# Kernel tuning notes

Measured on AMD Instinct MI355X. Metric: run time of the kernel, lower is better.

Reference implementation:

```python
import jax, jax.numpy as jnp
import numpy as np

N_TRIALS, T, N, IN_DIM = 32, 2048, 512, 64
DT = 0.1


def setup_inputs() -> dict:
    key = jax.random.key(0)
    k1, k2, k3, k4, k5 = jax.random.split(key, 5)
    inp = jax.random.normal(k1, (N_TRIALS, T, IN_DIM), dtype=jnp.float32)
    noise = jax.random.normal(k2, (N_TRIALS, T, N), dtype=jnp.float32)
    J = jax.random.normal(k3, (N, N), dtype=jnp.float32) * (1.0 / np.sqrt(N))  # init_std/sqrt(N)
    B = jax.random.normal(k4, (N, IN_DIM), dtype=jnp.float32)
    sig = jax.random.uniform(k5, (N,), dtype=jnp.float32, minval=0.1, maxval=1.0)
    W = jnp.eye(N, dtype=jnp.float32)  # module sets W = torch.eye(N)
    return {"inp": inp, "noise": noise, "J": J, "B": B, "sig": sig, "W": W}


def reference(inp, noise, J, B, sig, W):
    n_trials = inp.shape[0]
    n = J.shape[0]
    x0 = jnp.zeros((n_trials, n), dtype=inp.dtype)  # initial_state=None -> zeros
    sqdt = DT ** 0.5
    sig2 = sig * sig
    inp_t = jnp.swapaxes(inp, 0, 1)      # (T, n_trials, input_dim)
    noise_t = jnp.swapaxes(noise, 0, 1)  # (T, n_trials, N)

    def step(x, ue):
        u, eps = ue
        x_new = (1.0 - DT) * x + DT * (jnp.tanh(x) @ J.T + u @ B.T) + sqdt * (eps * sig2)
        y = jnp.tanh(x_new) @ W
        return x_new, (x_new, y)

    _, (xs, ys) = jax.lax.scan(step, x0, (inp_t, noise_t))
    x_seq = jnp.concatenate([x0[:, None, :], jnp.swapaxes(xs, 0, 1)], axis=1)  # (n_trials, T+1, N)
    output_seq = jnp.swapaxes(ys, 0, 1)  # (n_trials, T, N)
    return x_seq, output_seq
```

## Files before the change

kernel.cpp:

```cpp
#include <hip/hip_runtime.h>
#include <stdint.h>


#define T_STEPS 2048
#define N_NEUR  512
#define IN_DIM  64

typedef __attribute__((ext_vector_type(8))) short bf16x8;
typedef __attribute__((ext_vector_type(4))) short short4v;
typedef __attribute__((ext_vector_type(4))) float f32x4;

__device__ __forceinline__ short f2bf(float x) {
    union { float f; uint32_t u; } v; v.f = x;
    uint32_t r = v.u + 0x7fffu + ((v.u >> 16) & 1u);
    return (short)(r >> 16);
}
__device__ __forceinline__ float bf2f(short s) {
    union { float f; uint32_t u; } v;
    v.u = ((uint32_t)(uint16_t)s) << 16;
    return v.f;
}

__device__ __forceinline__ int th_idx(int trial, int k) {
    int byte = trial * 1024 + k * 2;
    byte ^= (trial & 7) << 4;
    return byte >> 1;
}
__device__ __forceinline__ int u_idx(int trial, int d) {
    int byte = trial * 128 + d * 2;
    byte ^= (trial & 7) << 4;
    return byte >> 1;
}

__launch_bounds__(256, 1)
__global__ void rnn_main(const float* __restrict__ inp,
                         const float* __restrict__ noise,
                         const float* __restrict__ Jm,
                         const float* __restrict__ Bm,
                         const float* __restrict__ sig,
                         float* __restrict__ out_x,
                         float* __restrict__ out_y,
                         uint64_t* __restrict__ xch)
{
    const int tid  = threadIdx.x;
    const int lane = tid & 63;
    const int w    = tid >> 6;
    const int s    = blockIdx.x & 7;
    const int h    = blockIdx.x >> 3;
    const int i0   = s * 4;
    const int nbase = h * 256 + w * 64;
    const int li   = lane & 15;
    const int lk   = lane >> 4;

    __shared__ short th[16 * 512];
    __shared__ short uhi[16 * 64];
    __shared__ short ulo[16 * 64];

    {
        bf16x8 z = {0,0,0,0,0,0,0,0};
        for (int j = tid; j < (16*512)/8; j += 256) *(bf16x8*)&th[j*8] = z;
        for (int j = tid; j < (16*64)/8;  j += 256) { *(bf16x8*)&uhi[j*8] = z; *(bf16x8*)&ulo[j*8] = z; }
    }

    bf16x8 Jf[4][16];
    #pragma unroll
    for (int mt = 0; mt < 4; ++mt) {
        const float* rowp = Jm + (size_t)(nbase + 16*mt + li) * N_NEUR;
        #pragma unroll
        for (int kt = 0; kt < 16; ++kt) {
            const float* p = rowp + kt*32 + lk*8;
            f32x4 a = *(const f32x4*)p;
            f32x4 b = *(const f32x4*)(p + 4);
            bf16x8 f;
            f[0]=f2bf(a[0]); f[1]=f2bf(a[1]); f[2]=f2bf(a[2]); f[3]=f2bf(a[3]);
            f[4]=f2bf(b[0]); f[5]=f2bf(b[1]); f[6]=f2bf(b[2]); f[7]=f2bf(b[3]);
            Jf[mt][kt] = f;
        }
    }

    bf16x8 Bhi[4][2], Blo[4][2];
    #pragma unroll
    for (int mt = 0; mt < 4; ++mt) {
        const float* rowp = Bm + (size_t)(nbase + 16*mt + li) * IN_DIM;
        #pragma unroll
        for (int kt2 = 0; kt2 < 2; ++kt2) {
            const float* p = rowp + kt2*32 + lk*8;
            f32x4 a = *(const f32x4*)p;
            f32x4 b = *(const f32x4*)(p + 4);
            bf16x8 fh, fl;
            #pragma unroll
            for (int e = 0; e < 4; ++e) {
                short hi = f2bf(a[e]); fh[e]   = hi; fl[e]   = f2bf(a[e] - bf2f(hi));
                short h2 = f2bf(b[e]); fh[e+4] = h2; fl[e+4] = f2bf(b[e] - bf2f(h2));
            }
            Bhi[mt][kt2] = fh; Blo[mt][kt2] = fl;
        }
    }

    const float SQDT = 0.316227766016837933f;
    f32x4 s2[4];
    #pragma unroll
    for (int mt = 0; mt < 4; ++mt) {
        int n4 = nbase + 16*mt + lk*4;
        #pragma unroll
        for (int r = 0; r < 4; ++r) { float sg = sig[n4 + r]; s2[mt][r] = SQDT * sg * sg; }
    }

    f32x4 x[4];
    #pragma unroll
    for (int mt = 0; mt < 4; ++mt) x[mt] = f32x4{0.f,0.f,0.f,0.f};

    const bool act  = (li < 4);
    const int trial = i0 + li;
    const int i_stage = tid >> 6;
    const int d_stage = tid & 63;

    {
        float v = inp[((size_t)(i0 + i_stage) * T_STEPS + 0) * IN_DIM + d_stage];
        short hi = f2bf(v);
        short lo = f2bf(v - bf2f(hi));
        uhi[u_idx(i_stage, d_stage)] = hi;
        ulo[u_idx(i_stage, d_stage)] = lo;
    }
    f32x4 noise_cur[4];
    #pragma unroll
    for (int mt = 0; mt < 4; ++mt) noise_cur[mt] = f32x4{0.f,0.f,0.f,0.f};
    if (act) {
        #pragma unroll
        for (int mt = 0; mt < 4; ++mt) {
            int n4 = nbase + 16*mt + lk*4;
            noise_cur[mt] = *(const f32x4*)&noise[((size_t)trial * T_STEPS + 0) * N_NEUR + n4];
        }
    }
    __syncthreads();

    for (int t = 0; t < T_STEPS; ++t) {
        const bool more = (t < T_STEPS - 1);

        float inp_next = 0.f;
        f32x4 noise_next[4];
        if (more) {
            inp_next = inp[((size_t)(i0 + i_stage) * T_STEPS + (t+1)) * IN_DIM + d_stage];
            if (act) {
                #pragma unroll
                for (int mt = 0; mt < 4; ++mt) {
                    int n4 = nbase + 16*mt + lk*4;
                    noise_next[mt] = *(const f32x4*)&noise[((size_t)trial * T_STEPS + (t+1)) * N_NEUR + n4];
                }
            }
        }

        f32x4 acc[4];
        #pragma unroll
        for (int mt = 0; mt < 4; ++mt) acc[mt] = f32x4{0.f,0.f,0.f,0.f};

        #pragma unroll
        for (int kt2 = 0; kt2 < 2; ++kt2) {
            bf16x8 uh = *(const bf16x8*)&uhi[u_idx(li, kt2*32 + lk*8)];
            bf16x8 ul = *(const bf16x8*)&ulo[u_idx(li, kt2*32 + lk*8)];
            #pragma unroll
            for (int mt = 0; mt < 4; ++mt) {
                acc[mt] = __builtin_amdgcn_mfma_f32_16x16x32_bf16(Bhi[mt][kt2], uh, acc[mt], 0, 0, 0);
                acc[mt] = __builtin_amdgcn_mfma_f32_16x16x32_bf16(Blo[mt][kt2], uh, acc[mt], 0, 0, 0);
                acc[mt] = __builtin_amdgcn_mfma_f32_16x16x32_bf16(Bhi[mt][kt2], ul, acc[mt], 0, 0, 0);
            }
        }
        #pragma unroll
        for (int kt = 0; kt < 16; ++kt) {
            bf16x8 bf = *(const bf16x8*)&th[th_idx(li, kt*32 + lk*8)];
            #pragma unroll
            for (int mt = 0; mt < 4; ++mt)
                acc[mt] = __builtin_amdgcn_mfma_f32_16x16x32_bf16(Jf[mt][kt], bf, acc[mt], 0, 0, 0);
        }

        __syncthreads();

        const uint32_t tag = (uint32_t)(t + 1);
        const uint64_t tag2 = ((uint64_t)tag << 32) | ((uint64_t)tag << 48);
        uint64_t* own_slot = xch + ((((t & 1) * 16) + s*2 + h) << 9);

        #pragma unroll
        for (int mt = 0; mt < 4; ++mt) {
            int n4 = nbase + 16*mt + lk*4;
            f32x4 xn, tv;
            #pragma unroll
            for (int r = 0; r < 4; ++r) {
                xn[r] = 0.9f * x[mt][r] + 0.1f * acc[mt][r] + noise_cur[mt][r] * s2[mt][r];
                float e = __expf(2.0f * xn[r]);
                tv[r] = 1.0f - 2.0f / (e + 1.0f);
            }
            x[mt] = xn;
            if (act) {
                *(f32x4*)&out_x[((size_t)trial * (T_STEPS+1) + (t+1)) * N_NEUR + n4] = xn;
                *(f32x4*)&out_y[((size_t)trial * T_STEPS + t) * N_NEUR + n4] = tv;
                short4v pk;
                pk[0]=f2bf(tv[0]); pk[1]=f2bf(tv[1]); pk[2]=f2bf(tv[2]); pk[3]=f2bf(tv[3]);
                *(short4v*)&th[th_idx(li, n4)] = pk;
                if (more) {
                    int nl = n4 - h*256;
                    uint64_t w0 = (uint64_t)(uint16_t)pk[0] | ((uint64_t)(uint16_t)pk[1] << 16) | tag2;
                    uint64_t w1 = (uint64_t)(uint16_t)pk[2] | ((uint64_t)(uint16_t)pk[3] << 16) | tag2;
                    uint64_t* dst = own_slot + li*128 + (nl >> 1);
                    __hip_atomic_store(dst,     w0, __ATOMIC_RELAXED, __HIP_MEMORY_SCOPE_AGENT);
                    __hip_atomic_store(dst + 1, w1, __ATOMIC_RELAXED, __HIP_MEMORY_SCOPE_AGENT);
                }
            }
        }

        if (more) {
            {
                short hi = f2bf(inp_next);
                short lo = f2bf(inp_next - bf2f(hi));
                uhi[u_idx(i_stage, d_stage)] = hi;
                ulo[u_idx(i_stage, d_stage)] = lo;
            }
            {
                const uint64_t* src = xch + ((((t & 1) * 16) + s*2 + (h^1)) << 9)
                                          + i_stage*128 + d_stage*2;
                const uint32_t want_hi = tag | (tag << 16);
                uint64_t w0, w1;
                for (;;) {
                    w0 = __hip_atomic_load(src,     __ATOMIC_RELAXED, __HIP_MEMORY_SCOPE_AGENT);
                    w1 = __hip_atomic_load(src + 1, __ATOMIC_RELAXED, __HIP_MEMORY_SCOPE_AGENT);
                    if ((uint32_t)(w0 >> 32) == want_hi && (uint32_t)(w1 >> 32) == want_hi) break;
                    __builtin_amdgcn_s_sleep(1);
                }
                short4v pv;
                pv[0] = (short)(w0 & 0xffff); pv[1] = (short)((w0 >> 16) & 0xffff);
                pv[2] = (short)(w1 & 0xffff); pv[3] = (short)((w1 >> 16) & 0xffff);
                *(short4v*)&th[th_idx(i_stage, (h^1)*256 + d_stage*4)] = pv;
            }
            #pragma unroll
            for (int mt = 0; mt < 4; ++mt) noise_cur[mt] = noise_next[mt];
            __syncthreads();
        }
    }
}

__global__ void init_kernel(float* __restrict__ out_x, uint64_t* __restrict__ xch) {
    int tid = blockIdx.x * 256 + threadIdx.x;
    if (tid < 2*8*2*512)
        __hip_atomic_store(&xch[tid], 0ull, __ATOMIC_RELAXED, __HIP_MEMORY_SCOPE_AGENT);
    if (tid < 32 * N_NEUR) {
        int i = tid >> 9;
        int n = tid & 511;
        out_x[(size_t)i * ((size_t)(T_STEPS+1) * N_NEUR) + n] = 0.0f;
    }
}

extern "C" void kernel_launch(void* const* d_in, const int* in_sizes, int n_in,
                              void* d_out, int out_size, void* d_ws, size_t ws_size,
                              hipStream_t stream) {
    const float* inp   = (const float*)d_in[0];
    const float* noise = (const float*)d_in[1];
    const float* Jm    = (const float*)d_in[2];
    const float* Bm    = (const float*)d_in[3];
    const float* sig   = (const float*)d_in[4];

    float* out_x = (float*)d_out;
    float* out_y = out_x + (size_t)32 * (T_STEPS+1) * N_NEUR;

    uint64_t* xch = (uint64_t*)d_ws;

    init_kernel<<<64, 256, 0, stream>>>(out_x, xch);
    rnn_main<<<16, 256, 0, stream>>>(inp, noise, Jm, Bm, sig, out_x, out_y, xch);
}
```

Before: 6.072 ms.

## Repartition RNN across 8-block trial groups with double-buffered LDS exchange

Changes the work split so each block handles all 16 trials of one group for a 64-neuron slice, with 8 blocks per group exchanging tanh activations through tagged global slots. Previously each block covered 4 trials and 256 neurons, and 12 of the 16 MFMA columns were padding. The new split uses all 16 MFMA columns, cuts per-wave MFMA count and register-held J to a quarter, and double-buffers the shared th/u arrays to remove one barrier per step. In exchange, each step now needs a 7-way all-gather across blocks instead of a 2-way exchange, which raises synchronization latency and global traffic on the serial critical path.

```diff
diff --git a/kernel.cpp b/kernel.cpp
--- a/kernel.cpp
+++ b/kernel.cpp
@@ -30,6 +30,13 @@
     int byte = trial * 128 + d * 2;
     byte ^= (trial & 7) << 4;
     return byte >> 1;
+}
+
+__device__ __forceinline__ uint64_t aload(const uint64_t* p) {
+    return __hip_atomic_load(p, __ATOMIC_RELAXED, __HIP_MEMORY_SCOPE_AGENT);
+}
+__device__ __forceinline__ void astore(uint64_t* p, uint64_t v) {
+    __hip_atomic_store(p, v, __ATOMIC_RELAXED, __HIP_MEMORY_SCOPE_AGENT);
 }
 
 __launch_bounds__(256, 1)
@@ -44,28 +51,28 @@
 {
     const int tid  = threadIdx.x;
     const int lane = tid & 63;
-    const int w    = tid >> 6;
-    const int s    = blockIdx.x & 7;
-    const int h    = blockIdx.x >> 3;
-    const int i0   = s * 4;
-    const int nbase = h * 256 + w * 64;
+    const int wv   = tid >> 6;
+    const int g    = blockIdx.x >> 3;
+    const int slo  = blockIdx.x & 7;
     const int li   = lane & 15;
     const int lk   = lane >> 4;
-
-    __shared__ short th[16 * 512];
-    __shared__ short uhi[16 * 64];
-    __shared__ short ulo[16 * 64];
+    const int n0   = slo * 64 + wv * 16;
+    const int trial = g * 16 + li;
+    const int n4   = n0 + lk * 4;
+
+    __shared__ short th[2][16 * 512];
+    __shared__ short uhi[2][16 * 64];
+    __shared__ short ulo[2][16 * 64];
 
     {
         bf16x8 z = {0,0,0,0,0,0,0,0};
-        for (int j = tid; j < (16*512)/8; j += 256) *(bf16x8*)&th[j*8] = z;
-        for (int j = tid; j < (16*64)/8;  j += 256) { *(bf16x8*)&uhi[j*8] = z; *(bf16x8*)&ulo[j*8] = z; }
-    }
-
-    bf16x8 Jf[4][16];
-    #pragma unroll
-    for (int mt = 0; mt < 4; ++mt) {
-        const float* rowp = Jm + (size_t)(nbase + 16*mt + li) * N_NEUR;
+        short* thp = &th[0][0];
+        for (int j = tid; j < (2*16*512)/8; j += 256) *(bf16x8*)&thp[j*8] = z;
+    }
+
+    bf16x8 Jf[16];
+    {
+        const float* rowp = Jm + (size_t)(n0 + li) * N_NEUR;
         #pragma unroll
         for (int kt = 0; kt < 16; ++kt) {
             const float* p = rowp + kt*32 + lk*8;
@@ -74,14 +81,13 @@
             bf16x8 f;
             f[0]=f2bf(a[0]); f[1]=f2bf(a[1]); f[2]=f2bf(a[2]); f[3]=f2bf(a[3]);
             f[4]=f2bf(b[0]); f[5]=f2bf(b[1]); f[6]=f2bf(b[2]); f[7]=f2bf(b[3]);
-            Jf[mt][kt] = f;
-        }
-    }
-
-    bf16x8 Bhi[4][2], Blo[4][2];
-    #pragma unroll
-    for (int mt = 0; mt < 4; ++mt) {
-        const float* rowp = Bm + (size_t)(nbase + 16*mt + li) * IN_DIM;
+            Jf[kt] = f;
+        }
+    }
+
+    bf16x8 Bhi[2], Blo[2];
+    {
+        const float* rowp = Bm + (size_t)(n0 + li) * IN_DIM;
         #pragma unroll
         for (int kt2 = 0; kt2 < 2; ++kt2) {
             const float* p = rowp + kt2*32 + lk*8;
@@ -90,157 +96,152 @@
             bf16x8 fh, fl;
             #pragma unroll
             for (int e = 0; e < 4; ++e) {
-                short hi = f2bf(a[e]); fh[e]   = hi; fl[e]   = f2bf(a[e] - bf2f(hi));
+                short h1 = f2bf(a[e]); fh[e]   = h1; fl[e]   = f2bf(a[e] - bf2f(h1));
                 short h2 = f2bf(b[e]); fh[e+4] = h2; fl[e+4] = f2bf(b[e] - bf2f(h2));
             }
-            Bhi[mt][kt2] = fh; Blo[mt][kt2] = fl;
+            Bhi[kt2] = fh; Blo[kt2] = fl;
         }
     }
 
     const float SQDT = 0.316227766016837933f;
-    f32x4 s2[4];
+    f32x4 s2;
     #pragma unroll
-    for (int mt = 0; mt < 4; ++mt) {
-        int n4 = nbase + 16*mt + lk*4;
-        #pragma unroll
-        for (int r = 0; r < 4; ++r) { float sg = sig[n4 + r]; s2[mt][r] = SQDT * sg * sg; }
-    }
-
-    f32x4 x[4];
-    #pragma unroll
-    for (int mt = 0; mt < 4; ++mt) x[mt] = f32x4{0.f,0.f,0.f,0.f};
-
-    const bool act  = (li < 4);
-    const int trial = i0 + li;
-    const int i_stage = tid >> 6;
-    const int d_stage = tid & 63;
-
-    {
-        float v = inp[((size_t)(i0 + i_stage) * T_STEPS + 0) * IN_DIM + d_stage];
-        short hi = f2bf(v);
-        short lo = f2bf(v - bf2f(hi));
-        uhi[u_idx(i_stage, d_stage)] = hi;
-        ulo[u_idx(i_stage, d_stage)] = lo;
-    }
-    f32x4 noise_cur[4];
-    #pragma unroll
-    for (int mt = 0; mt < 4; ++mt) noise_cur[mt] = f32x4{0.f,0.f,0.f,0.f};
-    if (act) {
-        #pragma unroll
-        for (int mt = 0; mt < 4; ++mt) {
-            int n4 = nbase + 16*mt + lk*4;
-            noise_cur[mt] = *(const f32x4*)&noise[((size_t)trial * T_STEPS + 0) * N_NEUR + n4];
-        }
-    }
+    for (int r = 0; r < 4; ++r) { float sg = sig[n4 + r]; s2[r] = SQDT * sg * sg; }
+
+    f32x4 x = f32x4{0.f, 0.f, 0.f, 0.f};
+
+    const int it  = tid >> 4;
+    const int c16 = tid & 15;
+    const int d4  = c16 * 4;
+
+    {
+        f32x4 uv = *(const f32x4*)&inp[((size_t)(g*16 + it) * T_STEPS + 0) * IN_DIM + d4];
+        short4v h, l;
+        #pragma unroll
+        for (int e = 0; e < 4; ++e) { h[e] = f2bf(uv[e]); l[e] = f2bf(uv[e] - bf2f(h[e])); }
+        *(short4v*)&uhi[0][u_idx(it, d4)] = h;
+        *(short4v*)&ulo[0][u_idx(it, d4)] = l;
+    }
+    f32x4 noise_cur = *(const f32x4*)&noise[((size_t)trial * T_STEPS + 0) * N_NEUR + n4];
     __syncthreads();
 
     for (int t = 0; t < T_STEPS; ++t) {
         const bool more = (t < T_STEPS - 1);
-
-        float inp_next = 0.f;
-        f32x4 noise_next[4];
-        if (more) {
-            inp_next = inp[((size_t)(i0 + i_stage) * T_STEPS + (t+1)) * IN_DIM + d_stage];
-            if (act) {
-                #pragma unroll
-                for (int mt = 0; mt < 4; ++mt) {
-                    int n4 = nbase + 16*mt + lk*4;
-                    noise_next[mt] = *(const f32x4*)&noise[((size_t)trial * T_STEPS + (t+1)) * N_NEUR + n4];
-                }
-            }
-        }
-
-        f32x4 acc[4];
-        #pragma unroll
-        for (int mt = 0; mt < 4; ++mt) acc[mt] = f32x4{0.f,0.f,0.f,0.f};
-
+        const int rp = t & 1, wp = rp ^ 1, par = t & 1;
+
+        f32x4 inp_next = f32x4{0.f,0.f,0.f,0.f};
+        f32x4 noise_next = f32x4{0.f,0.f,0.f,0.f};
+        if (more) {
+            inp_next = *(const f32x4*)&inp[((size_t)(g*16 + it) * T_STEPS + (t+1)) * IN_DIM + d4];
+            noise_next = *(const f32x4*)&noise[((size_t)trial * T_STEPS + (t+1)) * N_NEUR + n4];
+        }
+
+        f32x4 acc = f32x4{0.f,0.f,0.f,0.f};
         #pragma unroll
         for (int kt2 = 0; kt2 < 2; ++kt2) {
-            bf16x8 uh = *(const bf16x8*)&uhi[u_idx(li, kt2*32 + lk*8)];
-            bf16x8 ul = *(const bf16x8*)&ulo[u_idx(li, kt2*32 + lk*8)];
-            #pragma unroll
-            for (int mt = 0; mt < 4; ++mt) {
-                acc[mt] = __builtin_amdgcn_mfma_f32_16x16x32_bf16(Bhi[mt][kt2], uh, acc[mt], 0, 0, 0);
-                acc[mt] = __builtin_amdgcn_mfma_f32_16x16x32_bf16(Blo[mt][kt2], uh, acc[mt], 0, 0, 0);
-                acc[mt] = __builtin_amdgcn_mfma_f32_16x16x32_bf16(Bhi[mt][kt2], ul, acc[mt], 0, 0, 0);
-            }
+            bf16x8 uh = *(const bf16x8*)&uhi[rp][u_idx(li, kt2*32 + lk*8)];
+            bf16x8 ul = *(const bf16x8*)&ulo[rp][u_idx(li, kt2*32 + lk*8)];
+            acc = __builtin_amdgcn_mfma_f32_16x16x32_bf16(Bhi[kt2], uh, acc, 0, 0, 0);
+            acc = __builtin_amdgcn_mfma_f32_16x16x32_bf16(Blo[kt2], uh, acc, 0, 0, 0);
+            acc = __builtin_amdgcn_mfma_f32_16x16x32_bf16(Bhi[kt2], ul, acc, 0, 0, 0);
         }
         #pragma unroll
         for (int kt = 0; kt < 16; ++kt) {
-            bf16x8 bf = *(const bf16x8*)&th[th_idx(li, kt*32 + lk*8)];
-            #pragma unroll
-            for (int mt = 0; mt < 4; ++mt)
-                acc[mt] = __builtin_amdgcn_mfma_f32_16x16x32_bf16(Jf[mt][kt], bf, acc[mt], 0, 0, 0);
-        }
-
-        __syncthreads();
+            bf16x8 bf = *(const bf16x8*)&th[rp][th_idx(li, kt*32 + lk*8)];
+            acc = __builtin_amdgcn_mfma_f32_16x16x32_bf16(Jf[kt], bf, acc, 0, 0, 0);
+        }
+
+        f32x4 xn, tv;
+        #pragma unroll
+        for (int r = 0; r < 4; ++r) {
+            xn[r] = 0.9f * x[r] + 0.1f * acc[r] + noise_cur[r] * s2[r];
+            float e = __expf(2.0f * xn[r]);
+            tv[r] = 1.0f - 2.0f / (e + 1.0f);
+        }
+        x = xn;
+
+        short4v pk;
+        #pragma unroll
+        for (int r = 0; r < 4; ++r) pk[r] = f2bf(tv[r]);
 
         const uint32_t tag = (uint32_t)(t + 1);
         const uint64_t tag2 = ((uint64_t)tag << 32) | ((uint64_t)tag << 48);
-        uint64_t* own_slot = xch + ((((t & 1) * 16) + s*2 + h) << 9);
-
-        #pragma unroll
-        for (int mt = 0; mt < 4; ++mt) {
-            int n4 = nbase + 16*mt + lk*4;
-            f32x4 xn, tv;
+        const uint32_t want = tag | (tag << 16);
+
+        if (more) {
+            uint64_t w0 = (uint64_t)(uint16_t)pk[0] | ((uint64_t)(uint16_t)pk[1] << 16) | tag2;
+            uint64_t w1 = (uint64_t)(uint16_t)pk[2] | ((uint64_t)(uint16_t)pk[3] << 16) | tag2;
+            uint64_t* dst = xch + (((par*2 + g)*8 + slo) << 9) + li*32 + wv*8 + lk*2;
+            astore(dst,     w0);
+            astore(dst + 1, w1);
+        }
+
+        uint64_t v0[7], v1[7];
+        if (more) {
             #pragma unroll
-            for (int r = 0; r < 4; ++r) {
-                xn[r] = 0.9f * x[mt][r] + 0.1f * acc[mt][r] + noise_cur[mt][r] * s2[mt][r];
-                float e = __expf(2.0f * xn[r]);
-                tv[r] = 1.0f - 2.0f / (e + 1.0f);
-            }
-            x[mt] = xn;
-            if (act) {
-                *(f32x4*)&out_x[((size_t)trial * (T_STEPS+1) + (t+1)) * N_NEUR + n4] = xn;
-                *(f32x4*)&out_y[((size_t)trial * T_STEPS + t) * N_NEUR + n4] = tv;
-                short4v pk;
-                pk[0]=f2bf(tv[0]); pk[1]=f2bf(tv[1]); pk[2]=f2bf(tv[2]); pk[3]=f2bf(tv[3]);
-                *(short4v*)&th[th_idx(li, n4)] = pk;
-                if (more) {
-                    int nl = n4 - h*256;
-                    uint64_t w0 = (uint64_t)(uint16_t)pk[0] | ((uint64_t)(uint16_t)pk[1] << 16) | tag2;
-                    uint64_t w1 = (uint64_t)(uint16_t)pk[2] | ((uint64_t)(uint16_t)pk[3] << 16) | tag2;
-                    uint64_t* dst = own_slot + li*128 + (nl >> 1);
-                    __hip_atomic_store(dst,     w0, __ATOMIC_RELAXED, __HIP_MEMORY_SCOPE_AGENT);
-                    __hip_atomic_store(dst + 1, w1, __ATOMIC_RELAXED, __HIP_MEMORY_SCOPE_AGENT);
+            for (int s = 0; s < 7; ++s) {
+                int sl = s + (s >= slo ? 1 : 0);
+                const uint64_t* src = xch + (((par*2 + g)*8 + sl) << 9) + it*32 + c16*2;
+                v0[s] = aload(src);
+                v1[s] = aload(src + 1);
+            }
+        }
+
+        *(short4v*)&th[wp][th_idx(li, n4)] = pk;
+
+        *(f32x4*)&out_x[((size_t)trial * (T_STEPS+1) + (t+1)) * N_NEUR + n4] = xn;
+        *(f32x4*)&out_y[((size_t)trial * T_STEPS + t) * N_NEUR + n4] = tv;
+
+        if (more) {
+            {
+                short4v h, l;
+                #pragma unroll
+                for (int e = 0; e < 4; ++e) { h[e] = f2bf(inp_next[e]); l[e] = f2bf(inp_next[e] - bf2f(h[e])); }
+                *(short4v*)&uhi[wp][u_idx(it, d4)] = h;
+                *(short4v*)&ulo[wp][u_idx(it, d4)] = l;
+            }
+
+            uint32_t mask = 0x7f;
+            #pragma unroll
+            for (int s = 0; s < 7; ++s) {
+                int sl = s + (s >= slo ? 1 : 0);
+                if ((uint32_t)(v0[s] >> 32) == want && (uint32_t)(v1[s] >> 32) == want) {
+                    short4v pv;
+                    pv[0] = (short)(v0[s] & 0xffff); pv[1] = (short)((v0[s] >> 16) & 0xffff);
+                    pv[2] = (short)(v1[s] & 0xffff); pv[3] = (short)((v1[s] >> 16) & 0xffff);
+                    *(short4v*)&th[wp][th_idx(it, sl*64 + d4)] = pv;
+                    mask &= ~(1u << s);
                 }
             }
-        }
-
-        if (more) {
-            {
-                short hi = f2bf(inp_next);
-                short lo = f2bf(inp_next - bf2f(hi));
-                uhi[u_idx(i_stage, d_stage)] = hi;
-                ulo[u_idx(i_stage, d_stage)] = lo;
-            }
-            {
-                const uint64_t* src = xch + ((((t & 1) * 16) + s*2 + (h^1)) << 9)
-                                          + i_stage*128 + d_stage*2;
-                const uint32_t want_hi = tag | (tag << 16);
-                uint64_t w0, w1;
-                for (;;) {
-                    w0 = __hip_atomic_load(src,     __ATOMIC_RELAXED, __HIP_MEMORY_SCOPE_AGENT);
-                    w1 = __hip_atomic_load(src + 1, __ATOMIC_RELAXED, __HIP_MEMORY_SCOPE_AGENT);
-                    if ((uint32_t)(w0 >> 32) == want_hi && (uint32_t)(w1 >> 32) == want_hi) break;
-                    __builtin_amdgcn_s_sleep(1);
+            while (mask) {
+                #pragma unroll
+                for (int s = 0; s < 7; ++s) {
+                    if (mask & (1u << s)) {
+                        int sl = s + (s >= slo ? 1 : 0);
+                        const uint64_t* src = xch + (((par*2 + g)*8 + sl) << 9) + it*32 + c16*2;
+                        uint64_t a = aload(src);
+                        uint64_t b = aload(src + 1);
+                        if ((uint32_t)(a >> 32) == want && (uint32_t)(b >> 32) == want) {
+                            short4v pv;
+                            pv[0] = (short)(a & 0xffff); pv[1] = (short)((a >> 16) & 0xffff);
+                            pv[2] = (short)(b & 0xffff); pv[3] = (short)((b >> 16) & 0xffff);
+                            *(short4v*)&th[wp][th_idx(it, sl*64 + d4)] = pv;
+                            mask &= ~(1u << s);
+                        }
+                    }
                 }
-                short4v pv;
-                pv[0] = (short)(w0 & 0xffff); pv[1] = (short)((w0 >> 16) & 0xffff);
-                pv[2] = (short)(w1 & 0xffff); pv[3] = (short)((w1 >> 16) & 0xffff);
-                *(short4v*)&th[th_idx(i_stage, (h^1)*256 + d_stage*4)] = pv;
-            }
-            #pragma unroll
-            for (int mt = 0; mt < 4; ++mt) noise_cur[mt] = noise_next[mt];
-            __syncthreads();
-        }
+            }
+            noise_cur = noise_next;
+        }
+
+        __syncthreads();
     }
 }
 
 __global__ void init_kernel(float* __restrict__ out_x, uint64_t* __restrict__ xch) {
     int tid = blockIdx.x * 256 + threadIdx.x;
-    if (tid < 2*8*2*512)
-        __hip_atomic_store(&xch[tid], 0ull, __ATOMIC_RELAXED, __HIP_MEMORY_SCOPE_AGENT);
+    if (tid < 2*2*8*512)
+        astore(&xch[tid], 0ull);
     if (tid < 32 * N_NEUR) {
         int i = tid >> 9;
         int n = tid & 511;
```

After: 6.689 ms. +10.2%, slower.

## Pack 16 trials per block and overlap partner exchange with own-half matmul

Applied to the files above, without the earlier changes.

Only 4 blocks now do the work: each block pair covers 16 trials instead of 4, so all MFMA columns hold useful trials rather than 4 of 16. The J matmul is split into the block's own half, computed while the partner's half is loaded, and the partner's half, computed after the exchange. Double-buffered LDS removes one barrier per step. A startup ping test picks sc0 or sc0|sc1 cache bits for the exchange traffic. The cost is 4x more trials per block on each serial step, plus inline asm loads and stores whose coherence depends on the cache bits chosen.

```diff
diff --git a/kernel.cpp b/kernel.cpp
--- a/kernel.cpp
+++ b/kernel.cpp
@@ -5,10 +5,13 @@
 #define T_STEPS 2048
 #define N_NEUR  512
 #define IN_DIM  64
+#define HSQ     16384
+#define PING_ITERS 3000
 
 typedef __attribute__((ext_vector_type(8))) short bf16x8;
 typedef __attribute__((ext_vector_type(4))) short short4v;
 typedef __attribute__((ext_vector_type(4))) float f32x4;
+typedef __attribute__((ext_vector_type(4))) uint32_t u32x4;
 
 __device__ __forceinline__ short f2bf(float x) {
     union { float f; uint32_t u; } v; v.f = x;
@@ -30,6 +33,40 @@
     int byte = trial * 128 + d * 2;
     byte ^= (trial & 7) << 4;
     return byte >> 1;
+}
+
+__device__ __forceinline__ void xstore16(uint64_t* p, u32x4 v, bool s1) {
+    if (s1) asm volatile("global_store_dwordx4 %0, %1, off sc0 sc1" :: "v"(p), "v"(v) : "memory");
+    else    asm volatile("global_store_dwordx4 %0, %1, off sc0"     :: "v"(p), "v"(v) : "memory");
+}
+__device__ __forceinline__ void xissue64(const uint64_t* p, bool s1,
+                                         u32x4& a, u32x4& b, u32x4& c, u32x4& d) {
+    if (s1) asm volatile(
+        "global_load_dwordx4 %0, %4, off sc0 sc1\n\t"
+        "global_load_dwordx4 %1, %4, off offset:16 sc0 sc1\n\t"
+        "global_load_dwordx4 %2, %4, off offset:32 sc0 sc1\n\t"
+        "global_load_dwordx4 %3, %4, off offset:48 sc0 sc1"
+        : "=v"(a), "=v"(b), "=v"(c), "=v"(d) : "v"(p) : "memory");
+    else asm volatile(
+        "global_load_dwordx4 %0, %4, off sc0\n\t"
+        "global_load_dwordx4 %1, %4, off offset:16 sc0\n\t"
+        "global_load_dwordx4 %2, %4, off offset:32 sc0\n\t"
+        "global_load_dwordx4 %3, %4, off offset:48 sc0"
+        : "=v"(a), "=v"(b), "=v"(c), "=v"(d) : "v"(p) : "memory");
+}
+__device__ __forceinline__ void xwait(u32x4& a, u32x4& b, u32x4& c, u32x4& d) {
+    asm volatile("s_waitcnt vmcnt(0)"
+                 : "+v"(a), "+v"(b), "+v"(c), "+v"(d) :: "memory");
+    __builtin_amdgcn_sched_barrier(0);
+}
+__device__ __forceinline__ void ping_store(uint64_t* p, uint64_t v) {
+    asm volatile("global_store_dwordx2 %0, %1, off sc0" :: "v"(p), "v"(v) : "memory");
+}
+__device__ __forceinline__ uint64_t ping_load(const uint64_t* p) {
+    uint64_t v;
+    asm volatile("global_load_dwordx2 %0, %1, off sc0\n\ts_waitcnt vmcnt(0)"
+                 : "=v"(v) : "v"(p) : "memory");
+    return v;
 }
 
 __launch_bounds__(256, 1)
@@ -40,26 +77,33 @@
                          const float* __restrict__ sig,
                          float* __restrict__ out_x,
                          float* __restrict__ out_y,
-                         uint64_t* __restrict__ xch)
+                         uint64_t* __restrict__ xchq)
 {
+    const int bid = blockIdx.x;
+    if (!(bid == 0 || bid == 1 || bid == 8 || bid == 9)) return;
+
     const int tid  = threadIdx.x;
     const int lane = tid & 63;
-    const int w    = tid >> 6;
-    const int s    = blockIdx.x & 7;
-    const int h    = blockIdx.x >> 3;
-    const int i0   = s * 4;
-    const int nbase = h * 256 + w * 64;
+    const int wv   = tid >> 6;
+    const int g    = bid & 1;
+    const int h    = (bid >> 3) & 1;
+    const int wid  = g * 2 + h;
+    const int pwid = g * 2 + (h ^ 1);
     const int li   = lane & 15;
     const int lk   = lane >> 4;
-
-    __shared__ short th[16 * 512];
-    __shared__ short uhi[16 * 64];
-    __shared__ short ulo[16 * 64];
+    const int nbase = h * 256 + wv * 64;
+    const int trial = g * 16 + li;
+    const int kt_own = h * 8;
+    const int kt_par = 8 - kt_own;
+
+    __shared__ short th[2][16 * 512];
+    __shared__ short uhi[2][16 * 64];
+    __shared__ short ulo[2][16 * 64];
+    __shared__ int mode_sh;
 
     {
         bf16x8 z = {0,0,0,0,0,0,0,0};
-        for (int j = tid; j < (16*512)/8; j += 256) *(bf16x8*)&th[j*8] = z;
-        for (int j = tid; j < (16*64)/8;  j += 256) { *(bf16x8*)&uhi[j*8] = z; *(bf16x8*)&ulo[j*8] = z; }
+        for (int j = tid; j < (16*512)/8; j += 256) *(bf16x8*)&th[0][j*8] = z;
     }
 
     bf16x8 Jf[4][16];
@@ -90,7 +134,7 @@
             bf16x8 fh, fl;
             #pragma unroll
             for (int e = 0; e < 4; ++e) {
-                short hi = f2bf(a[e]); fh[e]   = hi; fl[e]   = f2bf(a[e] - bf2f(hi));
+                short h1 = f2bf(a[e]); fh[e]   = h1; fl[e]   = f2bf(a[e] - bf2f(h1));
                 short h2 = f2bf(b[e]); fh[e+4] = h2; fl[e+4] = f2bf(b[e] - bf2f(h2));
             }
             Bhi[mt][kt2] = fh; Blo[mt][kt2] = fl;
@@ -98,66 +142,86 @@
     }
 
     const float SQDT = 0.316227766016837933f;
-    f32x4 s2[4];
+    f32x4 s2[4], x[4];
     #pragma unroll
     for (int mt = 0; mt < 4; ++mt) {
         int n4 = nbase + 16*mt + lk*4;
         #pragma unroll
         for (int r = 0; r < 4; ++r) { float sg = sig[n4 + r]; s2[mt][r] = SQDT * sg * sg; }
-    }
-
-    f32x4 x[4];
-    #pragma unroll
-    for (int mt = 0; mt < 4; ++mt) x[mt] = f32x4{0.f,0.f,0.f,0.f};
-
-    const bool act  = (li < 4);
-    const int trial = i0 + li;
-    const int i_stage = tid >> 6;
-    const int d_stage = tid & 63;
+        x[mt] = f32x4{0.f,0.f,0.f,0.f};
+    }
+
+    if (tid == 0) {
+        uint64_t* hs = xchq + HSQ;
+        bool ok = true;
+        #pragma unroll
+        for (int r = 1; r <= 2; ++r) {
+            ping_store(hs + wid*32, (uint64_t)r);
+            bool seen = false;
+            for (int it = 0; it < PING_ITERS && !seen; ++it) {
+                if (ping_load(hs + pwid*32) == (uint64_t)r) seen = true;
+                else __builtin_amdgcn_s_sleep(2);
+            }
+            if (!seen) { ok = false; break; }
+        }
+        uint32_t* vd = (uint32_t*)(hs + 4*32);
+        __hip_atomic_store(vd + wid*64, ok ? 2u : 1u,
+                           __ATOMIC_RELAXED, __HIP_MEMORY_SCOPE_AGENT);
+        uint32_t pv;
+        do {
+            pv = __hip_atomic_load(vd + pwid*64, __ATOMIC_RELAXED, __HIP_MEMORY_SCOPE_AGENT);
+            if (!pv) __builtin_amdgcn_s_sleep(4);
+        } while (!pv);
+        mode_sh = (ok && pv == 2u) ? 0 : 1;
+    }
+
+    const int it  = tid >> 4;
+    const int c16 = tid & 15;
+    const int d4  = c16 * 4;
 
     {
-        float v = inp[((size_t)(i0 + i_stage) * T_STEPS + 0) * IN_DIM + d_stage];
-        short hi = f2bf(v);
-        short lo = f2bf(v - bf2f(hi));
-        uhi[u_idx(i_stage, d_stage)] = hi;
-        ulo[u_idx(i_stage, d_stage)] = lo;
+        f32x4 uv = *(const f32x4*)&inp[((size_t)(g*16 + it) * T_STEPS + 0) * IN_DIM + d4];
+        short4v hh, ll;
+        #pragma unroll
+        for (int e = 0; e < 4; ++e) { hh[e] = f2bf(uv[e]); ll[e] = f2bf(uv[e] - bf2f(hh[e])); }
+        *(short4v*)&uhi[0][u_idx(it, d4)] = hh;
+        *(short4v*)&ulo[0][u_idx(it, d4)] = ll;
     }
     f32x4 noise_cur[4];
     #pragma unroll
-    for (int mt = 0; mt < 4; ++mt) noise_cur[mt] = f32x4{0.f,0.f,0.f,0.f};
-    if (act) {
-        #pragma unroll
-        for (int mt = 0; mt < 4; ++mt) {
-            int n4 = nbase + 16*mt + lk*4;
-            noise_cur[mt] = *(const f32x4*)&noise[((size_t)trial * T_STEPS + 0) * N_NEUR + n4];
-        }
+    for (int mt = 0; mt < 4; ++mt) {
+        int n4 = nbase + 16*mt + lk*4;
+        noise_cur[mt] = *(const f32x4*)&noise[((size_t)trial * T_STEPS + 0) * N_NEUR + n4];
     }
     __syncthreads();
+    const bool sc1m = (mode_sh != 0);
+
+    u32x4 pa = {0,0,0,0}, pb = {0,0,0,0}, pc = {0,0,0,0}, pd = {0,0,0,0};
 
     for (int t = 0; t < T_STEPS; ++t) {
         const bool more = (t < T_STEPS - 1);
-
-        float inp_next = 0.f;
+        const int rp = t & 1, wp = rp ^ 1;
+
+        f32x4 inp_next = f32x4{0.f,0.f,0.f,0.f};
         f32x4 noise_next[4];
+        #pragma unroll
+        for (int mt = 0; mt < 4; ++mt) noise_next[mt] = f32x4{0.f,0.f,0.f,0.f};
         if (more) {
-            inp_next = inp[((size_t)(i0 + i_stage) * T_STEPS + (t+1)) * IN_DIM + d_stage];
-            if (act) {
-                #pragma unroll
-                for (int mt = 0; mt < 4; ++mt) {
-                    int n4 = nbase + 16*mt + lk*4;
-                    noise_next[mt] = *(const f32x4*)&noise[((size_t)trial * T_STEPS + (t+1)) * N_NEUR + n4];
-                }
+            inp_next = *(const f32x4*)&inp[((size_t)(g*16 + it) * T_STEPS + (t+1)) * IN_DIM + d4];
+            #pragma unroll
+            for (int mt = 0; mt < 4; ++mt) {
+                int n4 = nbase + 16*mt + lk*4;
+                noise_next[mt] = *(const f32x4*)&noise[((size_t)trial * T_STEPS + (t+1)) * N_NEUR + n4];
             }
         }
 
         f32x4 acc[4];
         #pragma unroll
         for (int mt = 0; mt < 4; ++mt) acc[mt] = f32x4{0.f,0.f,0.f,0.f};
-
         #pragma unroll
         for (int kt2 = 0; kt2 < 2; ++kt2) {
-            bf16x8 uh = *(const bf16x8*)&uhi[u_idx(li, kt2*32 + lk*8)];
-            bf16x8 ul = *(const bf16x8*)&ulo[u_idx(li, kt2*32 + lk*8)];
+            bf16x8 uh = *(const bf16x8*)&uhi[rp][u_idx(li, kt2*32 + lk*8)];
+            bf16x8 ul = *(const bf16x8*)&ulo[rp][u_idx(li, kt2*32 + lk*8)];
             #pragma unroll
             for (int mt = 0; mt < 4; ++mt) {
                 acc[mt] = __builtin_amdgcn_mfma_f32_16x16x32_bf16(Bhi[mt][kt2], uh, acc[mt], 0, 0, 0);
@@ -165,19 +229,49 @@
                 acc[mt] = __builtin_amdgcn_mfma_f32_16x16x32_bf16(Bhi[mt][kt2], ul, acc[mt], 0, 0, 0);
             }
         }
-        #pragma unroll
-        for (int kt = 0; kt < 16; ++kt) {
-            bf16x8 bf = *(const bf16x8*)&th[th_idx(li, kt*32 + lk*8)];
+
+        const uint32_t want = (uint32_t)t | ((uint32_t)t << 16);
+        const uint64_t* src = xchq + (((((t+1)&1)*2 + g)*2 + (h^1)) << 11)
+                                   + it*128 + c16*8;
+        if (t > 0) xissue64(src, sc1m, pa, pb, pc, pd);
+
+        #pragma unroll
+        for (int j = 0; j < 8; ++j) {
+            bf16x8 bf = *(const bf16x8*)&th[rp][th_idx(li, (kt_own + j)*32 + lk*8)];
             #pragma unroll
             for (int mt = 0; mt < 4; ++mt)
-                acc[mt] = __builtin_amdgcn_mfma_f32_16x16x32_bf16(Jf[mt][kt], bf, acc[mt], 0, 0, 0);
-        }
-
+                acc[mt] = __builtin_amdgcn_mfma_f32_16x16x32_bf16(Jf[mt][kt_own + j], bf, acc[mt], 0, 0, 0);
+        }
+
+        if (t > 0) {
+            xwait(pa, pb, pc, pd);
+            for (;;) {
+                bool ok = (pa[1]==want) & (pa[3]==want) & (pb[1]==want) & (pb[3]==want)
+                        & (pc[1]==want) & (pc[3]==want) & (pd[1]==want) & (pd[3]==want);
+                if (ok) break;
+                __builtin_amdgcn_s_sleep(1);
+                xissue64(src, sc1m, pa, pb, pc, pd);
+                xwait(pa, pb, pc, pd);
+            }
+            const int kb = (h^1)*256 + c16*16;
+            union { uint32_t d2[2]; short4v s4; } q;
+            q.d2[0] = pa[0]; q.d2[1] = pa[2]; *(short4v*)&th[rp][th_idx(it, kb + 0)]  = q.s4;
+            q.d2[0] = pb[0]; q.d2[1] = pb[2]; *(short4v*)&th[rp][th_idx(it, kb + 4)]  = q.s4;
+            q.d2[0] = pc[0]; q.d2[1] = pc[2]; *(short4v*)&th[rp][th_idx(it, kb + 8)]  = q.s4;
+            q.d2[0] = pd[0]; q.d2[1] = pd[2]; *(short4v*)&th[rp][th_idx(it, kb + 12)] = q.s4;
+        }
         __syncthreads();
 
-        const uint32_t tag = (uint32_t)(t + 1);
-        const uint64_t tag2 = ((uint64_t)tag << 32) | ((uint64_t)tag << 48);
-        uint64_t* own_slot = xch + ((((t & 1) * 16) + s*2 + h) << 9);
+        #pragma unroll
+        for (int j = 0; j < 8; ++j) {
+            bf16x8 bf = *(const bf16x8*)&th[rp][th_idx(li, (kt_par + j)*32 + lk*8)];
+            #pragma unroll
+            for (int mt = 0; mt < 4; ++mt)
+                acc[mt] = __builtin_amdgcn_mfma_f32_16x16x32_bf16(Jf[mt][kt_par + j], bf, acc[mt], 0, 0, 0);
+        }
+
+        const uint32_t tagw = (uint32_t)(t+1) | ((uint32_t)(t+1) << 16);
+        uint64_t* dst0 = xchq + ((((t&1)*2 + g)*2 + h) << 11) + li*128 + wv*32 + lk*2;
 
         #pragma unroll
         for (int mt = 0; mt < 4; ++mt) {
@@ -190,57 +284,41 @@
                 tv[r] = 1.0f - 2.0f / (e + 1.0f);
             }
             x[mt] = xn;
-            if (act) {
-                *(f32x4*)&out_x[((size_t)trial * (T_STEPS+1) + (t+1)) * N_NEUR + n4] = xn;
-                *(f32x4*)&out_y[((size_t)trial * T_STEPS + t) * N_NEUR + n4] = tv;
-                short4v pk;
-                pk[0]=f2bf(tv[0]); pk[1]=f2bf(tv[1]); pk[2]=f2bf(tv[2]); pk[3]=f2bf(tv[3]);
-                *(short4v*)&th[th_idx(li, n4)] = pk;
-                if (more) {
-                    int nl = n4 - h*256;
-                    uint64_t w0 = (uint64_t)(uint16_t)pk[0] | ((uint64_t)(uint16_t)pk[1] << 16) | tag2;
-                    uint64_t w1 = (uint64_t)(uint16_t)pk[2] | ((uint64_t)(uint16_t)pk[3] << 16) | tag2;
-                    uint64_t* dst = own_slot + li*128 + (nl >> 1);
-                    __hip_atomic_store(dst,     w0, __ATOMIC_RELAXED, __HIP_MEMORY_SCOPE_AGENT);
-                    __hip_atomic_store(dst + 1, w1, __ATOMIC_RELAXED, __HIP_MEMORY_SCOPE_AGENT);
-                }
-            }
+
+            uint32_t w01, w23;
+            asm("v_cvt_pk_bf16_f32 %0, %1, %2" : "=v"(w01) : "v"(tv[0]), "v"(tv[1]));
+            asm("v_cvt_pk_bf16_f32 %0, %1, %2" : "=v"(w23) : "v"(tv[2]), "v"(tv[3]));
+
+            union { uint32_t d2[2]; short4v s4; } q;
+            q.d2[0] = w01; q.d2[1] = w23;
+            *(short4v*)&th[wp][th_idx(li, n4)] = q.s4;
+
+            if (more) {
+                u32x4 pv = {w01, tagw, w23, tagw};
+                xstore16(dst0 + mt*8, pv, sc1m);
+            }
+            *(f32x4*)&out_x[((size_t)trial * (T_STEPS+1) + (t+1)) * N_NEUR + n4] = xn;
+            *(f32x4*)&out_y[((size_t)trial * T_STEPS + t) * N_NEUR + n4] = tv;
         }
 
         if (more) {
-            {
-                short hi = f2bf(inp_next);
-                short lo = f2bf(inp_next - bf2f(hi));
-                uhi[u_idx(i_stage, d_stage)] = hi;
-                ulo[u_idx(i_stage, d_stage)] = lo;
-            }
-            {
-                const uint64_t* src = xch + ((((t & 1) * 16) + s*2 + (h^1)) << 9)
-                                          + i_stage*128 + d_stage*2;
-                const uint32_t want_hi = tag | (tag << 16);
-                uint64_t w0, w1;
-                for (;;) {
-                    w0 = __hip_atomic_load(src,     __ATOMIC_RELAXED, __HIP_MEMORY_SCOPE_AGENT);
-                    w1 = __hip_atomic_load(src + 1, __ATOMIC_RELAXED, __HIP_MEMORY_SCOPE_AGENT);
-                    if ((uint32_t)(w0 >> 32) == want_hi && (uint32_t)(w1 >> 32) == want_hi) break;
-                    __builtin_amdgcn_s_sleep(1);
-                }
-                short4v pv;
-                pv[0] = (short)(w0 & 0xffff); pv[1] = (short)((w0 >> 16) & 0xffff);
-                pv[2] = (short)(w1 & 0xffff); pv[3] = (short)((w1 >> 16) & 0xffff);
-                *(short4v*)&th[th_idx(i_stage, (h^1)*256 + d_stage*4)] = pv;
-            }
+            short4v hh, ll;
+            #pragma unroll
+            for (int e = 0; e < 4; ++e) { hh[e] = f2bf(inp_next[e]); ll[e] = f2bf(inp_next[e] - bf2f(hh[e])); }
+            *(short4v*)&uhi[wp][u_idx(it, d4)] = hh;
+            *(short4v*)&ulo[wp][u_idx(it, d4)] = ll;
             #pragma unroll
             for (int mt = 0; mt < 4; ++mt) noise_cur[mt] = noise_next[mt];
-            __syncthreads();
-        }
-    }
-}
-
-__global__ void init_kernel(float* __restrict__ out_x, uint64_t* __restrict__ xch) {
+        }
+
+        __syncthreads();
+    }
+}
+
+__global__ void init_kernel(float* __restrict__ out_x, uint64_t* __restrict__ xchq) {
     int tid = blockIdx.x * 256 + threadIdx.x;
-    if (tid < 2*8*2*512)
-        __hip_atomic_store(&xch[tid], 0ull, __ATOMIC_RELAXED, __HIP_MEMORY_SCOPE_AGENT);
+    for (int i = tid; i < HSQ + 640; i += 16384)
+        __hip_atomic_store(&xchq[i], 0ull, __ATOMIC_RELAXED, __HIP_MEMORY_SCOPE_AGENT);
     if (tid < 32 * N_NEUR) {
         int i = tid >> 9;
         int n = tid & 511;
@@ -260,8 +338,8 @@
     float* out_x = (float*)d_out;
     float* out_y = out_x + (size_t)32 * (T_STEPS+1) * N_NEUR;
 
-    uint64_t* xch = (uint64_t*)d_ws;
-
-    init_kernel<<<64, 256, 0, stream>>>(out_x, xch);
-    rnn_main<<<16, 256, 0, stream>>>(inp, noise, Jm, Bm, sig, out_x, out_y, xch);
-}
+    uint64_t* xchq = (uint64_t*)d_ws;
+
+    init_kernel<<<64, 256, 0, stream>>>(out_x, xchq);
+    rnn_main<<<16, 256, 0, stream>>>(inp, noise, Jm, Bm, sig, out_x, out_y, xchq);
+}
```

Measured after the change: 20.85 ms. +243.3%, slower.
